# Kernel optimization log

Measured on AMD Instinct MI355X. Metric: run time of the kernel, lower is better.

The kernel has to match this reference:

```python
import jax, jax.numpy as jnp
import numpy as np

B, N, C, K = 2, 8192, 128, 16
EPS = 1e-5


def setup_inputs() -> dict:
    key = jax.random.key(0)
    ks = jax.random.split(key, 24)
    s = 1.0 / np.sqrt(C)
    nrm = lambda k, shape, sc: jax.random.normal(k, shape, dtype=jnp.float32) * sc
    return {
        "xyz": jax.random.normal(ks[0], (B, N, 3), dtype=jnp.float32),
        "feat": jax.random.normal(ks[1], (B, N, C), dtype=jnp.float32),
        "Wq": nrm(ks[2], (C, C), s),
        "Wk": nrm(ks[3], (C, C), s),
        "Wv": nrm(ks[4], (C, C), s),
        "pW1": nrm(ks[5], (C, 3), 0.5),
        "pb1": nrm(ks[6], (C,), 0.1),
        "pg": jnp.ones((C,), jnp.float32),
        "pbeta": jnp.zeros((C,), jnp.float32),
        "pmean": nrm(ks[7], (C,), 0.1),
        "pvar": jax.random.uniform(ks[8], (C,), jnp.float32, 0.5, 1.5),
        "pW2": nrm(ks[9], (C, C), s),
        "pb2": nrm(ks[10], (C,), 0.1),
        "aW1": nrm(ks[11], (C, C), s),
        "ab1": nrm(ks[12], (C,), 0.1),
        "ag": jnp.ones((C,), jnp.float32),
        "abeta": jnp.zeros((C,), jnp.float32),
        "amean": nrm(ks[13], (C,), 0.1),
        "avar": jax.random.uniform(ks[14], (C,), jnp.float32, 0.5, 1.5),
        "aW2": nrm(ks[15], (C, C), s),
        "ab2": nrm(ks[16], (C,), 0.1),
        "Wout": nrm(ks[17], (C, C), s),
    }


def _bn(x, g, b, mean, var):
    # eval-mode BatchNorm1d with running stats
    return (x - mean) * jax.lax.rsqrt(var + EPS) * g + b


def _lin(x, W):
    # torch nn.Linear convention: W is [out, in]
    return jnp.einsum('...i,oi->...o', x, W)


def reference(xyz, feat, Wq, Wk, Wv, pW1, pb1, pg, pbeta, pmean, pvar, pW2, pb2,
              aW1, ab1, ag, abeta, amean, avar, aW2, ab2, Wout):
    # KNN via squared distances (||a||^2 + ||b||^2 - 2 a.b), [B,N,N]
    sq = jnp.sum(xyz * xyz, axis=-1)
    dist = sq[:, :, None] + sq[:, None, :] - 2.0 * jnp.einsum('bnd,bmd->bnm', xyz, xyz)
    _, idx = jax.lax.top_k(-dist, K)  # [B,N,K] nearest neighbors

    gather = jax.vmap(lambda pts, i: pts[i])  # [B,N,C],[B,N,K] -> [B,N,K,C]
    nb_xyz = gather(xyz, idx)    # [B,N,K,3]
    nb_feat = gather(feat, idx)  # [B,N,K,C]

    q = _lin(feat, Wq)[:, :, None, :]  # [B,N,1,C]
    k = _lin(nb_feat, Wk)              # [B,N,K,C]
    v = _lin(nb_feat, Wv)              # [B,N,K,C]

    rel = nb_xyz - xyz[:, :, None, :]  # [B,N,K,3]
    pos = _lin(jax.nn.relu(_bn(_lin(rel, pW1) + pb1, pg, pbeta, pmean, pvar)), pW2) + pb2

    attn = q - k + pos
    attn = _lin(jax.nn.relu(_bn(_lin(attn, aW1) + ab1, ag, abeta, amean, avar)), aW2) + ab2
    attn = jax.nn.softmax(attn, axis=2)  # per-channel softmax over K neighbors

    out = jnp.sum(attn * (v + pos), axis=2)  # [B,N,C]
    return _lin(out, Wout)
```

## Files before the change

### kernel.cpp

```cpp
#include <hip/hip_runtime.h>
#include <cstdint>
#include <cstddef>

#define BB 2
#define NN 8192
#define CC 128
#define KK 16
#define EPSV 1e-5f
#define GRP 8
#define GPTS 1024
#define GCAP 60

typedef unsigned long long u64;
typedef unsigned int u32;
typedef unsigned short ushort_t;
typedef short short8v __attribute__((ext_vector_type(8)));
typedef float f32x4 __attribute__((ext_vector_type(4)));

__device__ __forceinline__ float med3f(float x, float y, float z) {
  float r;
  asm("v_med3_f32 %0, %1, %2, %3" : "=v"(r) : "v"(x), "v"(y), "v"(z));
  return r;
}

__global__ __launch_bounds__(256) void k_prep(const float* __restrict__ xyz,
                                              float4* __restrict__ xyzw) {
  int t = blockIdx.x * 256 + threadIdx.x;
  if (t >= BB * NN) return;
  float x = xyz[t * 3 + 0], y = xyz[t * 3 + 1], z = xyz[t * 3 + 2];
  float sq = __fadd_rn(__fadd_rn(__fmul_rn(x, x), __fmul_rn(y, y)), __fmul_rn(z, z));
  xyzw[t] = make_float4(x, y, z, sq);
}

__device__ __forceinline__ float distf(const float4& q, const float4& c) {
  float dot = __fadd_rn(__fadd_rn(__fmul_rn(q.x, c.x), __fmul_rn(q.y, c.y)),
                        __fmul_rn(q.z, c.z));
  float d = __fsub_rn(__fadd_rn(q.w, c.w), __fmul_rn(2.0f, dot));
  return fmaxf(d, 0.0f);
}

__device__ __forceinline__ float distq(const float4& p, const float4& c) {
  return fmaf(p.z, c.z, fmaf(p.y, c.y, fmaf(p.x, c.x, p.w + c.w)));
}

__global__ __launch_bounds__(256) void k_thr(const float4* __restrict__ xyzw,
                                             float* __restrict__ thr) {
  __shared__ float part[64][4][16];
  const int tid = threadIdx.x;
  const int qloc = tid & 63;
  const int s = tid >> 6;
  const int n = blockIdx.x * 64 + qloc;
  const int b = n >> 13;
  const float4 q = xyzw[n];
  const float4 p = make_float4(-2.f * q.x, -2.f * q.y, -2.f * q.z, q.w);
  const float4* base = xyzw + b * NN;
  float a[KK];
#pragma unroll
  for (int i = 0; i < KK; ++i) a[i] = 3.4e38f;
  const int j0 = s * 2048;
#pragma unroll 4
  for (int i = 0; i < 256; ++i) {
    const float4 c = base[j0 + i * 8];
    const float d = distq(p, c);
#pragma unroll
    for (int k = KK - 1; k >= 1; --k) a[k] = med3f(d, a[k - 1], a[k]);
    a[0] = fminf(d, a[0]);
  }
#pragma unroll
  for (int i = 0; i < KK; ++i) part[qloc][s][i] = a[i];
  __syncthreads();
  if (s == 0) {
#pragma unroll
    for (int ss = 1; ss < 4; ++ss)
#pragma unroll
      for (int i = 0; i < KK; ++i) {
        const float d = part[qloc][ss][i];
#pragma unroll
        for (int k = KK - 1; k >= 1; --k) a[k] = med3f(d, a[k - 1], a[k]);
        a[0] = fminf(d, a[0]);
      }
    const float t = a[KK - 1];
    thr[n] = t + (5e-4f + 4e-5f * fabsf(t));
  }
}

__global__ __launch_bounds__(256) void k_collect(const float4* __restrict__ xyzw,
                                                 const float* __restrict__ thr,
                                                 u32* __restrict__ cnt8,
                                                 u32* __restrict__ list) {
  __shared__ float4 pts[GPTS];
  const int tid = threadIdx.x;
  const int n = blockIdx.x * 256 + tid;
  const int b = n >> 13;
  const int g = blockIdx.y;
  const int m0 = g * GPTS;
#pragma unroll
  for (int i = 0; i < GPTS / 256; ++i) pts[i * 256 + tid] = xyzw[b * NN + m0 + i * 256 + tid];
  const float4 q = xyzw[n];
  const float4 p = make_float4(-2.f * q.x, -2.f * q.y, -2.f * q.z, q.w);
  const float tn = thr[n];
  __syncthreads();
  u32* seg = list + ((size_t)n * GRP + g) * GCAP;
  int cnt = 0;
#pragma unroll 4
  for (int mi = 0; mi < GPTS; ++mi) {
    const float d = distq(p, pts[mi]);
    if (d <= tn) {
      if (cnt < GCAP) seg[cnt] = (u32)(m0 + mi);
      ++cnt;
    }
  }
  cnt8[n * GRP + g] = (u32)cnt;
}

__global__ __launch_bounds__(256) void k_fin(const float4* __restrict__ xyzw,
                                             const u32* __restrict__ cnt8,
                                             const u32* __restrict__ list,
                                             int* __restrict__ idx) {
  __shared__ double part[64][3][16];
  const int tid = threadIdx.x;
  const int qloc = tid & 63;
  const int s = tid >> 6;
  const int n = blockIdx.x * 64 + qloc;
  const int b = n >> 13;
  const float4 q = xyzw[n];
  double keys[KK];
#pragma unroll
  for (int i = 0; i < KK; ++i) keys[i] = __longlong_as_double(0x7FEFFFFFFFFFFFFFLL);
#pragma unroll
  for (int gg = 0; gg < 2; ++gg) {
    const int g = s + gg * 4;
    const int cn = (int)cnt8[n * GRP + g];
    const int cl = (cn < GCAP) ? cn : GCAP;
    const u32* L = list + ((size_t)n * GRP + g) * GCAP;
    for (int j = 0; j < cl; ++j) {
      const u32 m = L[j];
      const float d = distf(q, xyzw[b * NN + m]);
      u64 kb_ = ((u64)__float_as_uint(d) << 32) | m;
      double kd = __longlong_as_double((long long)kb_);
      if (kd < keys[KK - 1]) {
#pragma unroll
        for (int i = 0; i < KK; ++i) {
          double lo = fmin(keys[i], kd);
          kd = fmax(keys[i], kd);
          keys[i] = lo;
        }
      }
    }
  }
  if (s > 0) {
#pragma unroll
    for (int i = 0; i < KK; ++i) part[qloc][s - 1][i] = keys[i];
  }
  __syncthreads();
  if (s == 0) {
#pragma unroll
    for (int ss = 0; ss < 3; ++ss)
#pragma unroll
      for (int i = 0; i < KK; ++i) {
        double kd = part[qloc][ss][i];
        if (kd < keys[KK - 1]) {
#pragma unroll
          for (int k = 0; k < KK; ++k) {
            double lo = fmin(keys[k], kd);
            kd = fmax(keys[k], kd);
            keys[k] = lo;
          }
        }
      }
    bool ovf = false;
#pragma unroll
    for (int g = 0; g < GRP; ++g) ovf |= (cnt8[n * GRP + g] > GCAP);
    if (ovf) {
#pragma unroll
      for (int i = 0; i < KK; ++i) keys[i] = __longlong_as_double(0x7FEFFFFFFFFFFFFFLL);
      for (int mi = 0; mi < NN; ++mi) {
        const float d = distf(q, xyzw[b * NN + mi]);
        u64 kb_ = ((u64)__float_as_uint(d) << 32) | (u32)mi;
        double kd = __longlong_as_double((long long)kb_);
        if (kd < keys[KK - 1]) {
#pragma unroll
          for (int k = 0; k < KK; ++k) {
            double lo = fmin(keys[k], kd);
            kd = fmax(keys[k], kd);
            keys[k] = lo;
          }
        }
      }
    }
#pragma unroll
    for (int j = 0; j < KK; ++j)
      idx[n * KK + j] = (int)((u64)__double_as_longlong(keys[j]) & 0xffffffffu);
  }
}

__global__ __launch_bounds__(128) void k_fold(const float* __restrict__ aW1,
                                              const float* __restrict__ Wq,
                                              const float* __restrict__ Wk,
                                              const float* __restrict__ pW2,
                                              const float* __restrict__ pb2,
                                              float* __restrict__ WqA,
                                              float* __restrict__ WkA,
                                              float* __restrict__ WpA,
                                              float* __restrict__ tvec) {
  const int bx = blockIdx.x;
  const int j = threadIdx.x;
  if (bx == 48) {
    float s = 0.f;
    for (int i = 0; i < 128; ++i) s = fmaf(aW1[j * 128 + i], pb2[i], s);
    tvec[j] = s;
    return;
  }
  const int mat = bx >> 4;
  const int c0 = (bx & 15) * 8;
  const float* S = (mat == 0) ? Wq : (mat == 1) ? Wk : pW2;
  float* D = (mat == 0) ? WqA : (mat == 1) ? WkA : WpA;
  float acc[8];
#pragma unroll
  for (int r = 0; r < 8; ++r) acc[r] = 0.f;
  for (int i = 0; i < 128; ++i) {
    float sv = S[i * 128 + j];
#pragma unroll
    for (int r = 0; r < 8; ++r) acc[r] = fmaf(aW1[(c0 + r) * 128 + i], sv, acc[r]);
  }
#pragma unroll
  for (int r = 0; r < 8; ++r) D[(c0 + r) * 128 + j] = acc[r];
}

__device__ __forceinline__ void splitf(float a, ushort_t& h, ushort_t& l) {
  u32 ab = __float_as_uint(a);
  h = (ushort_t)(ab >> 16);
  float hif = __uint_as_float(ab & 0xffff0000u);
  l = (ushort_t)(__float_as_uint(a - hif) >> 16);
}

__global__ __launch_bounds__(256) void k_packw(
    const float* __restrict__ S0, const float* __restrict__ S1,
    const float* __restrict__ S2, const float* __restrict__ S3,
    const float* __restrict__ S4, const float* __restrict__ S5,
    const float* __restrict__ S6, ushort_t* __restrict__ Phall,
    ushort_t* __restrict__ Plall) {
  const int bx = blockIdx.x;
  const int mat = bx >> 3;
  const int T = bx & 7;
  const float* S;
  switch (mat) {
    case 0: S = S0; break;
    case 1: S = S1; break;
    case 2: S = S2; break;
    case 3: S = S3; break;
    case 4: S = S4; break;
    case 5: S = S5; break;
    default: S = S6; break;
  }
  const int tid = threadIdx.x;
  const int s = tid >> 4;
  const int lr = tid & 15;
  const int c = T * 16 + lr;
  short8v vh, vl;
#pragma unroll
  for (int e = 0; e < 8; ++e) {
    ushort_t hh, ll;
    splitf(S[c * 128 + s * 8 + e], hh, ll);
    vh[e] = (short)hh;
    vl[e] = (short)ll;
  }
  const int po = mat * 16384 + T * 2048 + s * 128 + lr * 8;
  *(short8v*)&Phall[po] = vh;
  *(short8v*)&Plall[po] = vl;
}

template <int ITERS>
__device__ __forceinline__ void stage_rows(const float4* __restrict__ G4,
                                           ushort_t* Bh, ushort_t* Bl, int tid) {
#pragma unroll
  for (int i = 0; i < ITERS; ++i) {
    int f = i * 256 + tid;
    int r = f >> 5, k4 = f & 31;
    float4 v = G4[f];
    ushort_t h0, l0, h1, l1, h2, l2, h3, l3;
    splitf(v.x, h0, l0);
    splitf(v.y, h1, l1);
    splitf(v.z, h2, l2);
    splitf(v.w, h3, l3);
    int slot = k4 >> 1;
    int sub = (k4 & 1) * 4;
    int base = r * 128 + ((slot ^ (r & 15)) * 8) + sub;
    *(uint2*)&Bh[base] = make_uint2((u32)h0 | ((u32)h1 << 16), (u32)h2 | ((u32)h3 << 16));
    *(uint2*)&Bl[base] = make_uint2((u32)l0 | ((u32)l1 << 16), (u32)l2 | ((u32)l3 << 16));
  }
}

__device__ __forceinline__ void gemm64g(const ushort_t* ABh, const ushort_t* ABl,
                                        const ushort_t* __restrict__ Ph,
                                        const ushort_t* __restrict__ Pl,
                                        f32x4 acc[2][4], int tid) {
  const int l = tid & 63, wid = tid >> 6;
  const int wrow = wid >> 1, wcol = wid & 1;
  const int lq = l >> 4, lr = l & 15;
#pragma unroll
  for (int ks = 0; ks < 4; ++ks) {
    const int sw8 = (((ks * 4 + lq) ^ lr) * 8);
    short8v ah[2], al[2], wh[4], wl[4];
#pragma unroll
    for (int ct = 0; ct < 4; ++ct) {
      int off = (wcol * 4 + ct) * 2048 + (ks * 4 + lq) * 128 + lr * 8;
      wh[ct] = *(const short8v*)&Ph[off];
      wl[ct] = *(const short8v*)&Pl[off];
    }
#pragma unroll
    for (int rt = 0; rt < 2; ++rt) {
      int row = wrow * 32 + rt * 16 + lr;
      ah[rt] = *(const short8v*)&ABh[row * 128 + sw8];
      al[rt] = *(const short8v*)&ABl[row * 128 + sw8];
    }
    __builtin_amdgcn_s_setprio(1);
#pragma unroll
    for (int rt = 0; rt < 2; ++rt)
#pragma unroll
      for (int ct = 0; ct < 4; ++ct) {
        acc[rt][ct] = __builtin_amdgcn_mfma_f32_16x16x32_bf16(ah[rt], wh[ct], acc[rt][ct], 0, 0, 0);
        acc[rt][ct] = __builtin_amdgcn_mfma_f32_16x16x32_bf16(ah[rt], wl[ct], acc[rt][ct], 0, 0, 0);
        acc[rt][ct] = __builtin_amdgcn_mfma_f32_16x16x32_bf16(al[rt], wh[ct], acc[rt][ct], 0, 0, 0);
      }
    __builtin_amdgcn_s_setprio(0);
  }
}

template <int NW>
__global__ __launch_bounds__(256) void k_mms(const float* __restrict__ A,
                                             const ushort_t* __restrict__ Phall,
                                             const ushort_t* __restrict__ Plall,
                                             int m0, float* __restrict__ C0,
                                             float* __restrict__ C1,
                                             float* __restrict__ C2) {
  __shared__ ushort_t ABh[32 * 128], ABl[32 * 128];
  const int tid = threadIdx.x;
  const int Rbase = blockIdx.x * 32;
  stage_rows<4>((const float4*)(A + (size_t)Rbase * 128), ABh, ABl, tid);
  __syncthreads();
  const int l = tid & 63, wid = tid >> 6;
  const int lq = l >> 4, lr = l & 15;
  float* Cs[3] = {C0, C1, C2};
#pragma unroll
  for (int w = 0; w < NW; ++w) {
    const ushort_t* Ph = Phall + (size_t)(m0 + w) * 16384;
    const ushort_t* Pl = Plall + (size_t)(m0 + w) * 16384;
    f32x4 acc[2][2];
#pragma unroll
    for (int rt = 0; rt < 2; ++rt)
#pragma unroll
      for (int ct = 0; ct < 2; ++ct) acc[rt][ct] = (f32x4)0.f;
#pragma unroll
    for (int ks = 0; ks < 4; ++ks) {
      const int sw8 = (((ks * 4 + lq) ^ lr) * 8);
      short8v ah[2], al[2], wh[2], wl[2];
#pragma unroll
      for (int ct = 0; ct < 2; ++ct) {
        int off = (wid * 2 + ct) * 2048 + (ks * 4 + lq) * 128 + lr * 8;
        wh[ct] = *(const short8v*)&Ph[off];
        wl[ct] = *(const short8v*)&Pl[off];
      }
#pragma unroll
      for (int rt = 0; rt < 2; ++rt) {
        int row = rt * 16 + lr;
        ah[rt] = *(const short8v*)&ABh[row * 128 + sw8];
        al[rt] = *(const short8v*)&ABl[row * 128 + sw8];
      }
#pragma unroll
      for (int rt = 0; rt < 2; ++rt)
#pragma unroll
        for (int ct = 0; ct < 2; ++ct) {
          acc[rt][ct] = __builtin_amdgcn_mfma_f32_16x16x32_bf16(ah[rt], wh[ct], acc[rt][ct], 0, 0, 0);
          acc[rt][ct] = __builtin_amdgcn_mfma_f32_16x16x32_bf16(ah[rt], wl[ct], acc[rt][ct], 0, 0, 0);
          acc[rt][ct] = __builtin_amdgcn_mfma_f32_16x16x32_bf16(al[rt], wh[ct], acc[rt][ct], 0, 0, 0);
        }
    }
#pragma unroll
    for (int rt = 0; rt < 2; ++rt)
#pragma unroll
      for (int ct = 0; ct < 2; ++ct) {
        int c = (wid * 2 + ct) * 16 + lr;
#pragma unroll
        for (int reg = 0; reg < 4; ++reg) {
          int R = Rbase + rt * 16 + lq * 4 + reg;
          Cs[w][(size_t)R * 128 + c] = acc[rt][ct][reg];
        }
      }
  }
}

__global__ __launch_bounds__(256, 3) void k_fused(
    const float4* __restrict__ xyzw, const int* __restrict__ idx,
    const float* __restrict__ qbA, const float* __restrict__ kbA,
    const float* __restrict__ vb, const float* __restrict__ pW1,
    const float* __restrict__ pb1, const float* __restrict__ pg,
    const float* __restrict__ pbeta, const float* __restrict__ pm,
    const float* __restrict__ pv, const float* __restrict__ pb2,
    const float* __restrict__ ab1, const float* __restrict__ ag,
    const float* __restrict__ abeta, const float* __restrict__ am,
    const float* __restrict__ av, const float* __restrict__ ab2,
    const float* __restrict__ tvec, const ushort_t* __restrict__ Phall,
    const ushort_t* __restrict__ Plall, float* __restrict__ outb) {
  __shared__ ushort_t ABh[64 * 128], ABl[64 * 128];
  __shared__ float4 fW1[128];
  __shared__ float sA[128], tA[128], pB2[128], aB2[128];
  __shared__ int idxs[64];
  const int tid = threadIdx.x;
  const int Qbase = blockIdx.x * 4;
  const int b = Qbase >> 13;

  if (tid < 64) idxs[tid] = idx[Qbase * KK + tid];
  if (tid < 128) {
    int c = tid;
    float s1 = pg[c] / sqrtf(pv[c] + EPSV);
    fW1[c] = make_float4(pW1[c * 3] * s1, pW1[c * 3 + 1] * s1, pW1[c * 3 + 2] * s1,
                         (pb1[c] - pm[c]) * s1 + pbeta[c]);
    float s2 = ag[c] / sqrtf(av[c] + EPSV);
    sA[c] = s2;
    tA[c] = fmaf(s2, ab1[c] + tvec[c] - am[c], abeta[c]);
    pB2[c] = pb2[c];
    aB2[c] = ab2[c];
  }
  __syncthreads();

  {
    int r = tid >> 2, qq = tid & 3;
    int Q = Qbase + (r >> 4);
    int m = idxs[r];
    float4 pq = xyzw[Q];
    float4 pn = xyzw[b * NN + m];
    float rx = pn.x - pq.x, ry = pn.y - pq.y, rz = pn.z - pq.z;
#pragma unroll
    for (int g = 0; g < 4; ++g) {
      short8v vh, vl;
      int c0 = qq * 32 + g * 8;
#pragma unroll
      for (int e = 0; e < 8; ++e) {
        float4 w = fW1[c0 + e];
        float h = fmaxf(fmaf(rz, w.z, fmaf(ry, w.y, fmaf(rx, w.x, w.w))), 0.f);
        ushort_t hh, ll;
        splitf(h, hh, ll);
        vh[e] = (short)hh;
        vl[e] = (short)ll;
      }
      int sw = (c0 >> 3) ^ (r & 15);
      *(short8v*)&ABh[r * 128 + sw * 8] = vh;
      *(short8v*)&ABl[r * 128 + sw * 8] = vl;
    }
  }
  __syncthreads();

  const int l = tid & 63, wid = tid >> 6;
  const int wrow = wid >> 1, wcol = wid & 1;
  const int lq = l >> 4, lr = l & 15;

  f32x4 pos_[2][4], pa_[2][4];
#pragma unroll
  for (int rt = 0; rt < 2; ++rt)
#pragma unroll
    for (int ct = 0; ct < 4; ++ct) {
      pos_[rt][ct] = (f32x4)0.f;
      pa_[rt][ct] = (f32x4)0.f;
    }
  gemm64g(ABh, ABl, Phall, Plall, pos_, tid);
  gemm64g(ABh, ABl, Phall + 16384, Plall + 16384, pa_, tid);
  __syncthreads();

#pragma unroll
  for (int rt = 0; rt < 2; ++rt) {
    int qi_loc = wrow * 2 + rt;
    int Q = Qbase + qi_loc;
    int mr[4];
#pragma unroll
    for (int reg = 0; reg < 4; ++reg) mr[reg] = b * NN + idxs[qi_loc * 16 + lq * 4 + reg];
#pragma unroll
    for (int ct = 0; ct < 4; ++ct) {
      int c = wcol * 64 + ct * 16 + lr;
      float qv = qbA[(size_t)Q * 128 + c];
      float sc = sA[c], tc = tA[c];
#pragma unroll
      for (int reg = 0; reg < 4; ++reg) {
        float u = qv - kbA[(size_t)mr[reg] * 128 + c] + pa_[rt][ct][reg];
        float z = fmaxf(fmaf(u, sc, tc), 0.f);
        ushort_t hh, ll;
        splitf(z, hh, ll);
        int R15 = lq * 4 + reg;
        int row = wrow * 32 + rt * 16 + R15;
        int base = row * 128 + (((c >> 3) ^ R15) * 8) + (c & 7);
        ABh[base] = hh;
        ABl[base] = ll;
      }
    }
  }
  __syncthreads();

  f32x4 acc[2][4];
#pragma unroll
  for (int rt = 0; rt < 2; ++rt)
#pragma unroll
    for (int ct = 0; ct < 4; ++ct) acc[rt][ct] = (f32x4)0.f;
  gemm64g(ABh, ABl, Phall + 32768, Plall + 32768, acc, tid);

#pragma unroll
  for (int rt = 0; rt < 2; ++rt) {
    int qi_loc = wrow * 2 + rt;
    int Q = Qbase + qi_loc;
    int mr[4];
#pragma unroll
    for (int reg = 0; reg < 4; ++reg) mr[reg] = b * NN + idxs[qi_loc * 16 + lq * 4 + reg];
#pragma unroll
    for (int ct = 0; ct < 4; ++ct) {
      int c = wcol * 64 + ct * 16 + lr;
      float ab2v = aB2[c];
      float lg[4];
#pragma unroll
      for (int reg = 0; reg < 4; ++reg) lg[reg] = acc[rt][ct][reg] + ab2v;
      float mx = fmaxf(fmaxf(lg[0], lg[1]), fmaxf(lg[2], lg[3]));
      mx = fmaxf(mx, __shfl_xor(mx, 16));
      mx = fmaxf(mx, __shfl_xor(mx, 32));
      float s = 0.f, o = 0.f;
      float pb2v = pB2[c];
#pragma unroll
      for (int reg = 0; reg < 4; ++reg) {
        float e_ = expf(lg[reg] - mx);
        s += e_;
        float vv = vb[(size_t)mr[reg] * 128 + c] + pos_[rt][ct][reg] + pb2v;
        o = fmaf(e_, vv, o);
      }
      s += __shfl_xor(s, 16);
      s += __shfl_xor(s, 32);
      o += __shfl_xor(o, 16);
      o += __shfl_xor(o, 32);
      if (lq == 0) outb[(size_t)Q * 128 + c] = o / s;
    }
  }
}

extern "C" void kernel_launch(void* const* d_in, const int* in_sizes, int n_in,
                              void* d_out, int out_size, void* d_ws, size_t ws_size,
                              hipStream_t stream) {
  const float* xyz = (const float*)d_in[0];
  const float* feat = (const float*)d_in[1];
  const float* Wq = (const float*)d_in[2];
  const float* Wk = (const float*)d_in[3];
  const float* Wv = (const float*)d_in[4];
  const float* pW1 = (const float*)d_in[5];
  const float* pb1 = (const float*)d_in[6];
  const float* pg = (const float*)d_in[7];
  const float* pbeta = (const float*)d_in[8];
  const float* pmean = (const float*)d_in[9];
  const float* pvar = (const float*)d_in[10];
  const float* pW2 = (const float*)d_in[11];
  const float* pb2 = (const float*)d_in[12];
  const float* aW1 = (const float*)d_in[13];
  const float* ab1 = (const float*)d_in[14];
  const float* ag = (const float*)d_in[15];
  const float* abeta = (const float*)d_in[16];
  const float* amean = (const float*)d_in[17];
  const float* avar = (const float*)d_in[18];
  const float* aW2 = (const float*)d_in[19];
  const float* ab2 = (const float*)d_in[20];
  const float* Wout = (const float*)d_in[21];
  float* out = (float*)d_out;
  char* ws = (char*)d_ws;

  size_t off = 0;
  auto alloc = [&](size_t bytes) {
    size_t r = off;
    off += (bytes + 255) & ~(size_t)255;
    return r;
  };
  float4* xyzw = (float4*)(ws + alloc((size_t)BB * NN * 16));
  int* idx = (int*)(ws + alloc((size_t)BB * NN * KK * 4));
  size_t o_qb = alloc((size_t)BB * NN * CC * 4);
  size_t o_kb = alloc((size_t)BB * NN * CC * 4);
  size_t o_vb = alloc((size_t)BB * NN * CC * 4);
  size_t o_ob = alloc((size_t)BB * NN * CC * 4);
  float* qbA = (float*)(ws + o_qb);
  float* kbA = (float*)(ws + o_kb);
  float* vb = (float*)(ws + o_vb);
  float* outb = (float*)(ws + o_ob);
  u32* list = (u32*)(ws + o_qb);
  float* WqA = (float*)(ws + alloc(128 * 128 * 4));
  float* WkA = (float*)(ws + alloc(128 * 128 * 4));
  float* WpA = (float*)(ws + alloc(128 * 128 * 4));
  float* tvec = (float*)(ws + alloc(128 * 4));
  ushort_t* Phall = (ushort_t*)(ws + alloc(7 * 16384 * 2));
  ushort_t* Plall = (ushort_t*)(ws + alloc(7 * 16384 * 2));
  float* thrbuf = (float*)(ws + alloc((size_t)BB * NN * 4));
  u32* cnt8 = (u32*)(ws + alloc((size_t)BB * NN * GRP * 4));

  k_prep<<<(BB * NN) / 256, 256, 0, stream>>>(xyz, xyzw);
  k_fold<<<49, 128, 0, stream>>>(aW1, Wq, Wk, pW2, pb2, WqA, WkA, WpA, tvec);
  k_packw<<<56, 256, 0, stream>>>(pW2, WpA, aW2, WqA, WkA, Wv, Wout, Phall, Plall);

  k_thr<<<(BB * NN) / 64, 256, 0, stream>>>(xyzw, thrbuf);
  k_collect<<<dim3((BB * NN) / 256, GRP), 256, 0, stream>>>(xyzw, thrbuf, cnt8, list);
  k_fin<<<(BB * NN) / 64, 256, 0, stream>>>(xyzw, cnt8, list, idx);

  k_mms<3><<<(BB * NN) / 32, 256, 0, stream>>>(feat, Phall, Plall, 3, qbA, kbA, vb);

  k_fused<<<(BB * NN * KK) / 64, 256, 0, stream>>>(
      xyzw, idx, qbA, kbA, vb, pW1, pb1, pg, pbeta, pmean, pvar, pb2, ab1, ag,
      abeta, amean, avar, ab2, tvec, Phall, Plall, outb);

  k_mms<1><<<(BB * NN) / 32, 256, 0, stream>>>(outb, Phall, Plall, 6, out, nullptr,
                                               nullptr);
}
```

Measured before the change: 289.1 us.

## Split KNN and GEMM kernels across more blocks and prefetch gathered rows

k_thr and k_fin now give each query 16 threads instead of 4 and merge partial top-K lists in two levels, with four times as many blocks. k_mms handles 16 rows per block instead of 32, which doubles the grid. In k_fused the q/k rows are loaded before the position-MLP stage and the v rows before the second GEMM, so gather latency can overlap other work. This buys more parallelism and latency hiding at the cost of extra merge passes, more registers and reloading the weights more often.

```diff
diff --git a/kernel.cpp b/kernel.cpp
--- a/kernel.cpp
+++ b/kernel.cpp
@@ -45,11 +45,11 @@
 
 __global__ __launch_bounds__(256) void k_thr(const float4* __restrict__ xyzw,
                                              float* __restrict__ thr) {
-  __shared__ float part[64][4][16];
+  __shared__ float part[16][16][16];
   const int tid = threadIdx.x;
-  const int qloc = tid & 63;
-  const int s = tid >> 6;
-  const int n = blockIdx.x * 64 + qloc;
+  const int qloc = tid & 15;
+  const int s = tid >> 4;
+  const int n = blockIdx.x * 16 + qloc;
   const int b = n >> 13;
   const float4 q = xyzw[n];
   const float4 p = make_float4(-2.f * q.x, -2.f * q.y, -2.f * q.z, q.w);
@@ -57,10 +57,10 @@
   float a[KK];
 #pragma unroll
   for (int i = 0; i < KK; ++i) a[i] = 3.4e38f;
-  const int j0 = s * 2048;
+  const int j0 = s * 64;
 #pragma unroll 4
-  for (int i = 0; i < 256; ++i) {
-    const float4 c = base[j0 + i * 8];
+  for (int i = 0; i < 64; ++i) {
+    const float4 c = base[(j0 + i) * 8];
     const float d = distq(p, c);
 #pragma unroll
     for (int k = KK - 1; k >= 1; --k) a[k] = med3f(d, a[k - 1], a[k]);
@@ -68,6 +68,20 @@
   }
 #pragma unroll
   for (int i = 0; i < KK; ++i) part[qloc][s][i] = a[i];
+  __syncthreads();
+  if (s < 4) {
+#pragma unroll
+    for (int ss = 1; ss < 4; ++ss)
+#pragma unroll
+      for (int i = 0; i < KK; ++i) {
+        const float d = part[qloc][s + ss * 4][i];
+#pragma unroll
+        for (int k = KK - 1; k >= 1; --k) a[k] = med3f(d, a[k - 1], a[k]);
+        a[0] = fminf(d, a[0]);
+      }
+#pragma unroll
+    for (int i = 0; i < KK; ++i) part[qloc][s][i] = a[i];
+  }
   __syncthreads();
   if (s == 0) {
 #pragma unroll
@@ -117,48 +131,44 @@
                                              const u32* __restrict__ cnt8,
                                              const u32* __restrict__ list,
                                              int* __restrict__ idx) {
-  __shared__ double part[64][3][16];
+  __shared__ double part[16][16][16];
   const int tid = threadIdx.x;
-  const int qloc = tid & 63;
-  const int s = tid >> 6;
-  const int n = blockIdx.x * 64 + qloc;
+  const int qloc = tid & 15;
+  const int s = tid >> 4;
+  const int n = blockIdx.x * 16 + qloc;
   const int b = n >> 13;
   const float4 q = xyzw[n];
+  const int g = s >> 1;
+  const int h = s & 1;
+  const int cn = (int)cnt8[n * GRP + g];
+  const int cl = (cn < GCAP) ? cn : GCAP;
+  const u32* L = list + ((size_t)n * GRP + g) * GCAP;
   double keys[KK];
 #pragma unroll
   for (int i = 0; i < KK; ++i) keys[i] = __longlong_as_double(0x7FEFFFFFFFFFFFFFLL);
-#pragma unroll
-  for (int gg = 0; gg < 2; ++gg) {
-    const int g = s + gg * 4;
-    const int cn = (int)cnt8[n * GRP + g];
-    const int cl = (cn < GCAP) ? cn : GCAP;
-    const u32* L = list + ((size_t)n * GRP + g) * GCAP;
-    for (int j = 0; j < cl; ++j) {
-      const u32 m = L[j];
-      const float d = distf(q, xyzw[b * NN + m]);
-      u64 kb_ = ((u64)__float_as_uint(d) << 32) | m;
-      double kd = __longlong_as_double((long long)kb_);
-      if (kd < keys[KK - 1]) {
-#pragma unroll
-        for (int i = 0; i < KK; ++i) {
-          double lo = fmin(keys[i], kd);
-          kd = fmax(keys[i], kd);
-          keys[i] = lo;
-        }
-      }
-    }
-  }
-  if (s > 0) {
-#pragma unroll
-    for (int i = 0; i < KK; ++i) part[qloc][s - 1][i] = keys[i];
-  }
-  __syncthreads();
-  if (s == 0) {
-#pragma unroll
-    for (int ss = 0; ss < 3; ++ss)
+  for (int j = h; j < cl; j += 2) {
+    const u32 m = L[j];
+    const float d = distf(q, xyzw[b * NN + m]);
+    u64 kb_ = ((u64)__float_as_uint(d) << 32) | m;
+    double kd = __longlong_as_double((long long)kb_);
+    if (kd < keys[KK - 1]) {
 #pragma unroll
       for (int i = 0; i < KK; ++i) {
-        double kd = part[qloc][ss][i];
+        double lo = fmin(keys[i], kd);
+        kd = fmax(keys[i], kd);
+        keys[i] = lo;
+      }
+    }
+  }
+#pragma unroll
+  for (int i = 0; i < KK; ++i) part[qloc][s][i] = keys[i];
+  __syncthreads();
+  if (s < 4) {
+#pragma unroll
+    for (int ss = 1; ss < 4; ++ss)
+#pragma unroll
+      for (int i = 0; i < KK; ++i) {
+        double kd = part[qloc][s + ss * 4][i];
         if (kd < keys[KK - 1]) {
 #pragma unroll
           for (int k = 0; k < KK; ++k) {
@@ -168,9 +178,28 @@
           }
         }
       }
+#pragma unroll
+    for (int i = 0; i < KK; ++i) part[qloc][s][i] = keys[i];
+  }
+  __syncthreads();
+  if (s == 0) {
+#pragma unroll
+    for (int ss = 1; ss < 4; ++ss)
+#pragma unroll
+      for (int i = 0; i < KK; ++i) {
+        double kd = part[qloc][ss][i];
+        if (kd < keys[KK - 1]) {
+#pragma unroll
+          for (int k = 0; k < KK; ++k) {
+            double lo = fmin(keys[k], kd);
+            kd = fmax(keys[k], kd);
+            keys[k] = lo;
+          }
+        }
+      }
     bool ovf = false;
 #pragma unroll
-    for (int g = 0; g < GRP; ++g) ovf |= (cnt8[n * GRP + g] > GCAP);
+    for (int gg = 0; gg < GRP; ++gg) ovf |= (cnt8[n * GRP + gg] > GCAP);
     if (ovf) {
 #pragma unroll
       for (int i = 0; i < KK; ++i) keys[i] = __longlong_as_double(0x7FEFFFFFFFFFFFFFLL);
@@ -334,10 +363,10 @@
                                              int m0, float* __restrict__ C0,
                                              float* __restrict__ C1,
                                              float* __restrict__ C2) {
-  __shared__ ushort_t ABh[32 * 128], ABl[32 * 128];
+  __shared__ ushort_t ABh[16 * 128], ABl[16 * 128];
   const int tid = threadIdx.x;
-  const int Rbase = blockIdx.x * 32;
-  stage_rows<4>((const float4*)(A + (size_t)Rbase * 128), ABh, ABl, tid);
+  const int Rbase = blockIdx.x * 16;
+  stage_rows<2>((const float4*)(A + (size_t)Rbase * 128), ABh, ABl, tid);
   __syncthreads();
   const int l = tid & 63, wid = tid >> 6;
   const int lq = l >> 4, lr = l & 15;
@@ -346,47 +375,37 @@
   for (int w = 0; w < NW; ++w) {
     const ushort_t* Ph = Phall + (size_t)(m0 + w) * 16384;
     const ushort_t* Pl = Plall + (size_t)(m0 + w) * 16384;
-    f32x4 acc[2][2];
-#pragma unroll
-    for (int rt = 0; rt < 2; ++rt)
-#pragma unroll
-      for (int ct = 0; ct < 2; ++ct) acc[rt][ct] = (f32x4)0.f;
+    f32x4 acc[2];
+#pragma unroll
+    for (int ct = 0; ct < 2; ++ct) acc[ct] = (f32x4)0.f;
 #pragma unroll
     for (int ks = 0; ks < 4; ++ks) {
       const int sw8 = (((ks * 4 + lq) ^ lr) * 8);
-      short8v ah[2], al[2], wh[2], wl[2];
+      short8v ah, al, wh[2], wl[2];
 #pragma unroll
       for (int ct = 0; ct < 2; ++ct) {
         int off = (wid * 2 + ct) * 2048 + (ks * 4 + lq) * 128 + lr * 8;
         wh[ct] = *(const short8v*)&Ph[off];
         wl[ct] = *(const short8v*)&Pl[off];
       }
-#pragma unroll
-      for (int rt = 0; rt < 2; ++rt) {
-        int row = rt * 16 + lr;
-        ah[rt] = *(const short8v*)&ABh[row * 128 + sw8];
-        al[rt] = *(const short8v*)&ABl[row * 128 + sw8];
-      }
-#pragma unroll
-      for (int rt = 0; rt < 2; ++rt)
-#pragma unroll
-        for (int ct = 0; ct < 2; ++ct) {
-          acc[rt][ct] = __builtin_amdgcn_mfma_f32_16x16x32_bf16(ah[rt], wh[ct], acc[rt][ct], 0, 0, 0);
-          acc[rt][ct] = __builtin_amdgcn_mfma_f32_16x16x32_bf16(ah[rt], wl[ct], acc[rt][ct], 0, 0, 0);
-          acc[rt][ct] = __builtin_amdgcn_mfma_f32_16x16x32_bf16(al[rt], wh[ct], acc[rt][ct], 0, 0, 0);
-        }
-    }
-#pragma unroll
-    for (int rt = 0; rt < 2; ++rt)
+      ah = *(const short8v*)&ABh[lr * 128 + sw8];
+      al = *(const short8v*)&ABl[lr * 128 + sw8];
 #pragma unroll
       for (int ct = 0; ct < 2; ++ct) {
-        int c = (wid * 2 + ct) * 16 + lr;
-#pragma unroll
-        for (int reg = 0; reg < 4; ++reg) {
-          int R = Rbase + rt * 16 + lq * 4 + reg;
-          Cs[w][(size_t)R * 128 + c] = acc[rt][ct][reg];
-        }
-      }
+        acc[ct] = __builtin_amdgcn_mfma_f32_16x16x32_bf16(ah, wh[ct], acc[ct], 0, 0, 0);
+        acc[ct] = __builtin_amdgcn_mfma_f32_16x16x32_bf16(ah, wl[ct], acc[ct], 0, 0, 0);
+        acc[ct] = __builtin_amdgcn_mfma_f32_16x16x32_bf16(al, wh[ct], acc[ct], 0, 0, 0);
+      }
+    }
+#pragma unroll
+    for (int ct = 0; ct < 2; ++ct) {
+      int c = (wid * 2 + ct) * 16 + lr;
+#pragma unroll
+      for (int reg = 0; reg < 4; ++reg) {
+        int R = Rbase + lq * 4 + reg;
+        Cs[w][(size_t)R * 128 + c] = acc[ct][reg];
+      }
+    }
   }
 }
 
@@ -424,6 +443,31 @@
   }
   __syncthreads();
 
+  const int l = tid & 63, wid = tid >> 6;
+  const int wrow = wid >> 1, wcol = wid & 1;
+  const int lq = l >> 4, lr = l & 15;
+
+  int mrow[2][4];
+#pragma unroll
+  for (int rt = 0; rt < 2; ++rt)
+#pragma unroll
+    for (int reg = 0; reg < 4; ++reg)
+      mrow[rt][reg] = b * NN + idxs[(wrow * 2 + rt) * 16 + lq * 4 + reg];
+  float qpre[2][4], kpre[2][4][4];
+#pragma unroll
+  for (int rt = 0; rt < 2; ++rt) {
+    const float* qrow = qbA + (size_t)(Qbase + wrow * 2 + rt) * 128;
+#pragma unroll
+    for (int ct = 0; ct < 4; ++ct) qpre[rt][ct] = qrow[wcol * 64 + ct * 16 + lr];
+#pragma unroll
+    for (int reg = 0; reg < 4; ++reg) {
+      const float* krow = kbA + (size_t)mrow[rt][reg] * 128;
+#pragma unroll
+      for (int ct = 0; ct < 4; ++ct)
+        kpre[rt][reg][ct] = krow[wcol * 64 + ct * 16 + lr];
+    }
+  }
+
   {
     int r = tid >> 2, qq = tid & 3;
     int Q = Qbase + (r >> 4);
@@ -451,10 +495,6 @@
   }
   __syncthreads();
 
-  const int l = tid & 63, wid = tid >> 6;
-  const int wrow = wid >> 1, wcol = wid & 1;
-  const int lq = l >> 4, lr = l & 15;
-
   f32x4 pos_[2][4], pa_[2][4];
 #pragma unroll
   for (int rt = 0; rt < 2; ++rt)
@@ -469,19 +509,14 @@
 
 #pragma unroll
   for (int rt = 0; rt < 2; ++rt) {
-    int qi_loc = wrow * 2 + rt;
-    int Q = Qbase + qi_loc;
-    int mr[4];
-#pragma unroll
-    for (int reg = 0; reg < 4; ++reg) mr[reg] = b * NN + idxs[qi_loc * 16 + lq * 4 + reg];
 #pragma unroll
     for (int ct = 0; ct < 4; ++ct) {
       int c = wcol * 64 + ct * 16 + lr;
-      float qv = qbA[(size_t)Q * 128 + c];
+      float qv = qpre[rt][ct];
       float sc = sA[c], tc = tA[c];
 #pragma unroll
       for (int reg = 0; reg < 4; ++reg) {
-        float u = qv - kbA[(size_t)mr[reg] * 128 + c] + pa_[rt][ct][reg];
+        float u = qv - kpre[rt][reg][ct] + pa_[rt][ct][reg];
         float z = fmaxf(fmaf(u, sc, tc), 0.f);
         ushort_t hh, ll;
         splitf(z, hh, ll);
@@ -493,6 +528,17 @@
       }
     }
   }
+
+  float vpre[2][4][4];
+#pragma unroll
+  for (int rt = 0; rt < 2; ++rt)
+#pragma unroll
+    for (int reg = 0; reg < 4; ++reg) {
+      const float* vrow = vb + (size_t)mrow[rt][reg] * 128;
+#pragma unroll
+      for (int ct = 0; ct < 4; ++ct)
+        vpre[rt][reg][ct] = vrow[wcol * 64 + ct * 16 + lr];
+    }
   __syncthreads();
 
   f32x4 acc[2][4];
@@ -504,11 +550,7 @@
 
 #pragma unroll
   for (int rt = 0; rt < 2; ++rt) {
-    int qi_loc = wrow * 2 + rt;
-    int Q = Qbase + qi_loc;
-    int mr[4];
-#pragma unroll
-    for (int reg = 0; reg < 4; ++reg) mr[reg] = b * NN + idxs[qi_loc * 16 + lq * 4 + reg];
+    int Q = Qbase + wrow * 2 + rt;
 #pragma unroll
     for (int ct = 0; ct < 4; ++ct) {
       int c = wcol * 64 + ct * 16 + lr;
@@ -525,7 +567,7 @@
       for (int reg = 0; reg < 4; ++reg) {
         float e_ = expf(lg[reg] - mx);
         s += e_;
-        float vv = vb[(size_t)mr[reg] * 128 + c] + pos_[rt][ct][reg] + pb2v;
+        float vv = vpre[rt][reg][ct] + pos_[rt][ct][reg] + pb2v;
         o = fmaf(e_, vv, o);
       }
       s += __shfl_xor(s, 16);
@@ -595,16 +637,16 @@
   k_fold<<<49, 128, 0, stream>>>(aW1, Wq, Wk, pW2, pb2, WqA, WkA, WpA, tvec);
   k_packw<<<56, 256, 0, stream>>>(pW2, WpA, aW2, WqA, WkA, Wv, Wout, Phall, Plall);
 
-  k_thr<<<(BB * NN) / 64, 256, 0, stream>>>(xyzw, thrbuf);
+  k_thr<<<(BB * NN) / 16, 256, 0, stream>>>(xyzw, thrbuf);
   k_collect<<<dim3((BB * NN) / 256, GRP), 256, 0, stream>>>(xyzw, thrbuf, cnt8, list);
-  k_fin<<<(BB * NN) / 64, 256, 0, stream>>>(xyzw, cnt8, list, idx);
-
-  k_mms<3><<<(BB * NN) / 32, 256, 0, stream>>>(feat, Phall, Plall, 3, qbA, kbA, vb);
+  k_fin<<<(BB * NN) / 16, 256, 0, stream>>>(xyzw, cnt8, list, idx);
+
+  k_mms<3><<<(BB * NN) / 16, 256, 0, stream>>>(feat, Phall, Plall, 3, qbA, kbA, vb);
 
   k_fused<<<(BB * NN * KK) / 64, 256, 0, stream>>>(
       xyzw, idx, qbA, kbA, vb, pW1, pb1, pg, pbeta, pmean, pvar, pb2, ab1, ag,
       abeta, amean, avar, ab2, tvec, Phall, Plall, outb);
 
-  k_mms<1><<<(BB * NN) / 32, 256, 0, stream>>>(outb, Phall, Plall, 6, out, nullptr,
+  k_mms<1><<<(BB * NN) / 16, 256, 0, stream>>>(outb, Phall, Plall, 6, out, nullptr,
                                                nullptr);
 }
```

Result: slower. 322.1 us (+11.4%).
